# Kernel tuning notes

Hardware: AMD Instinct MI355X
Metric: run time of the kernel (lower is better)

## Reference

```python
import jax, jax.numpy as jnp
import numpy as np
import math

V, T, D, H, L, B = 50257, 1024, 768, 12, 6, 2
FF = 4 * D
HD = D // H

def layernorm(x, g, b, eps=1e-5):
    mu = jnp.mean(x, axis=-1, keepdims=True)
    var = jnp.var(x, axis=-1, keepdims=True)
    return (x - mu) * jax.lax.rsqrt(var + eps) * g + b

def new_gelu(x):
    # Faithful to the (buggy) NewGelu: tanh arg = sqrt(2/pi) * 0.044715 * x**4
    c = math.sqrt(2.0 / math.pi)
    return 0.5 * x * (1.0 + jnp.tanh(c * (x * 0.044715 * jnp.power(x, 3))))

def setup_inputs() -> dict:
    key = jax.random.key(0)
    ks = jax.random.split(key, 18)
    n = lambda k, shape, s=0.02: (jax.random.normal(k, shape, dtype=jnp.float32) * s)
    return {
        "ids": jax.random.randint(ks[0], (B, T), 0, V),
        "wte": n(ks[1], (V, D)),
        "wpe": n(ks[2], (T, D)),
        "W_qkv": n(ks[3], (L, D, 3 * D)),
        "b_qkv": jnp.zeros((L, 3 * D), jnp.float32),
        "W_o": n(ks[4], (L, D, D)),
        "b_o": jnp.zeros((L, D), jnp.float32),
        "ln1_g": jnp.ones((L, D), jnp.float32),
        "ln1_b": jnp.zeros((L, D), jnp.float32),
        "W1": n(ks[5], (L, D, FF)),
        "b1": jnp.zeros((L, FF), jnp.float32),
        "W2": n(ks[6], (L, FF, D)),
        "b2": jnp.zeros((L, D), jnp.float32),
        "lnf_g": jnp.ones((D,), jnp.float32),
        "lnf_b": jnp.zeros((D,), jnp.float32),
        "W_head": n(ks[7], (D, V)),
        "b_head": jnp.zeros((V,), jnp.float32),
    }

def reference(ids, wte, wpe, W_qkv, b_qkv, W_o, b_o, ln1_g, ln1_b,
              W1, b1, W2, b2, lnf_g, lnf_b, W_head, b_head):
    t = ids.shape[1]
    x = wte[ids] + wpe[:t][None]  # [B,T,D]
    scale = 1.0 / math.sqrt(HD)
    for l in range(L):
        qkv = x @ W_qkv[l] + b_qkv[l]                 # [B,T,3D]
        q, k, v = jnp.split(qkv, 3, axis=-1)
        q = q.reshape(-1, t, H, HD).transpose(0, 2, 1, 3)  # [B,H,T,hd]
        k = k.reshape(-1, t, H, HD).transpose(0, 2, 1, 3)
        v = v.reshape(-1, t, H, HD).transpose(0, 2, 1, 3)
        # NOTE: mask buffer is all-ones in the source, so NO causal masking.
        att = jax.nn.softmax(jnp.einsum('bhqd,bhkd->bhqk', q, k) * scale, axis=-1)
        y = jnp.einsum('bhqk,bhkd->bhqd', att, v)
        y = y.transpose(0, 2, 1, 3).reshape(-1, t, D)
        y = y @ W_o[l] + b_o[l]
        x = layernorm(y, ln1_g[l], ln1_b[l]) + x      # ln1 AFTER attn, per source
        h = new_gelu(x @ W1[l] + b1[l]) @ W2[l] + b2[l]  # ln2 unused, per source
        x = h + x
    x = layernorm(x, lnf_g, lnf_b)
    logits = x @ W_head + b_head
    return logits
```

## Files before the change

kernel.cpp:

```cpp
#include <hip/hip_runtime.h>
#include <hip/hip_bf16.h>
#include <math.h>
#include <stdint.h>

#define NL 6
#define NB 2
#define ST 1024
#define ND 768
#define NH 12
#define HD 64
#define NFF 3072
#define NV 50257
#define ND3 2304
#define NM (NB * ST)

typedef short bf16x4 __attribute__((ext_vector_type(4)));
typedef short bf16x8 __attribute__((ext_vector_type(8)));
typedef float f32x4  __attribute__((ext_vector_type(4)));

typedef __attribute__((address_space(3))) void as3_void;
typedef __attribute__((address_space(1))) void as1_void;

__device__ __forceinline__ void async_copy16(const void* g, void* lds) {
  __builtin_amdgcn_global_load_lds((const as1_void*)(uintptr_t)g,
                                   (as3_void*)(uint32_t)(uintptr_t)lds,
                                   16, 0, 0);
}

__device__ __forceinline__ unsigned short f2bf(float f) {
  union { float f; uint32_t u; } v; v.f = f;
  return (unsigned short)((v.u + 0x7fffu + ((v.u >> 16) & 1u)) >> 16);
}

__device__ __forceinline__ bf16x8 frag16(const unsigned short* p) {
  return *(const bf16x8*)p;
}

template <int N>
__device__ __forceinline__ void wait_vm_barrier() {
  if constexpr (N == 8)      asm volatile("s_waitcnt vmcnt(8)\n\ts_barrier" ::: "memory");
  else if constexpr (N == 6) asm volatile("s_waitcnt vmcnt(6)\n\ts_barrier" ::: "memory");
  else if constexpr (N == 5) asm volatile("s_waitcnt vmcnt(5)\n\ts_barrier" ::: "memory");
  else if constexpr (N == 4) asm volatile("s_waitcnt vmcnt(4)\n\ts_barrier" ::: "memory");
  else                       asm volatile("s_waitcnt vmcnt(0)\n\ts_barrier" ::: "memory");
}
__device__ __forceinline__ void lgkm_barrier() {
  asm volatile("s_waitcnt lgkmcnt(0)\n\ts_barrier" ::: "memory");
}

#define MFMA(a, b, c) __builtin_amdgcn_mfma_f32_16x16x32_bf16((a), (b), (c), 0, 0, 0)

__device__ __forceinline__ float gelu_buggy(float x) {
  const float c = 0.7978845608028654f;
  float x2 = x * x;
  return 0.5f * x * (1.0f + tanhf(c * 0.044715f * x2 * x2));
}

enum { EP_QKV = 0, EP_PROJ, EP_FF1, EP_FF2, EP_HEAD };

template <int EPI, int TM, int TN, int WN, int NW, int BK, int NBUF>
__global__ __launch_bounds__(NW * 64)
void gemm_bt(const unsigned short* __restrict__ A,
             const unsigned short* __restrict__ BT,
             const float* __restrict__ bias,
             float* __restrict__ Cf,
             unsigned short* __restrict__ Cb,
             const float* __restrict__ resid,
             unsigned short* __restrict__ vT,
             int M, int N, int K)
{
  constexpr int WM = NW / WN;
  constexpr int FM = TM / WM / 16;
  constexpr int FN = TN / WN / 16;
  constexpr int SL = BK / 8;
  constexpr int RS = (BK == 32) ? 1 : 0;
  constexpr int RPC = 1024 / (BK * 2);
  constexpr int CA = TM / RPC / NW;
  constexpr int CB = TN / RPC / NW;
  constexpr int LPT = CA + CB;
  constexpr int KK = BK / 32;
  constexpr int DEPTH = NBUF - 1;
  __shared__ __align__(16) unsigned short As[NBUF][TM * BK];
  __shared__ __align__(16) unsigned short Bs[NBUF][TN * BK];
  const int tid = threadIdx.x;
  const int w = tid >> 6, l = tid & 63;
  const int g = l >> 4, r = l & 15;
  const int wm = (w / WN) * (FM * 16);
  const int wn = (w % WN) * (FN * 16);

  const int nbx = gridDim.x;
  const int nwg = nbx * gridDim.y;
  int bid = blockIdx.y * nbx + blockIdx.x;
  if ((nwg & 7) == 0) bid = (bid & 7) * (nwg >> 3) + (bid >> 3);
  const int m0 = (bid % nbx) * TM, n0 = (bid / nbx) * TN;

  const int sr = l / (BK / 8);
  const int se = ((l & (SL - 1)) ^ ((sr >> RS) & (SL - 1))) * 8;
  long aoff[CA];
  long boff[CB];
#pragma unroll
  for (int c = 0; c < CA; ++c) {
    const int arow = (w * CA + c) * RPC + sr;
    aoff[c] = (long)(m0 + arow) * K + se;
  }
#pragma unroll
  for (int c = 0; c < CB; ++c) {
    int brow = n0 + (w * CB + c) * RPC + sr;
    if (brow > N - 1) brow = N - 1;
    boff[c] = (long)brow * K + se;
  }

  f32x4 acc[FM][FN] = {};

  auto stage = [&](int t, int buf) {
    const long k0 = (long)t * BK;
#pragma unroll
    for (int c = 0; c < CA; ++c)
      async_copy16(A + aoff[c] + k0, &As[buf][(w * CA + c) * 512]);
#pragma unroll
    for (int c = 0; c < CB; ++c)
      async_copy16(BT + boff[c] + k0, &Bs[buf][(w * CB + c) * 512]);
  };

  auto compute = [&](int buf) {
#pragma unroll
    for (int kk = 0; kk < KK; ++kk) {
      bf16x8 af[FM], bf[FN];
#pragma unroll
      for (int mi = 0; mi < FM; ++mi)
        af[mi] = frag16(&As[buf][(wm + mi * 16 + r) * BK +
                                 (((kk * 4 + g) ^ ((r >> RS) & (SL - 1))) * 8)]);
#pragma unroll
      for (int ni = 0; ni < FN; ++ni)
        bf[ni] = frag16(&Bs[buf][(wn + ni * 16 + r) * BK +
                                 (((kk * 4 + g) ^ ((r >> RS) & (SL - 1))) * 8)]);
      __builtin_amdgcn_s_setprio(1);
#pragma unroll
      for (int mi = 0; mi < FM; ++mi)
#pragma unroll
        for (int ni = 0; ni < FN; ++ni)
          acc[mi][ni] = MFMA(af[mi], bf[ni], acc[mi][ni]);
      __builtin_amdgcn_s_setprio(0);
    }
  };

  const int nt = K / BK;
  stage(0, 0);
  if (DEPTH == 2) stage(1, 1);
  int cur = 0, nxt = DEPTH;
  for (int t = 0; t < nt; ++t) {
    const bool have_next = (t + DEPTH) < nt;
    if (have_next) stage(t + DEPTH, nxt);
    if (have_next && DEPTH == 2)       wait_vm_barrier<2 * LPT>();
    else if (have_next || (DEPTH == 2 && t + 1 < nt)) wait_vm_barrier<LPT>();
    else                               wait_vm_barrier<0>();
    compute(cur);
    if (t + 1 < nt) lgkm_barrier();
    cur = (cur + 1 == NBUF) ? 0 : cur + 1;
    nxt = (nxt + 1 == NBUF) ? 0 : nxt + 1;
  }

#pragma unroll
  for (int mi = 0; mi < FM; ++mi) {
#pragma unroll
    for (int ni = 0; ni < FN; ++ni) {
      const int col = n0 + wn + ni * 16 + r;
      const float bb = bias[col];
      if (EPI == EP_QKV && col >= 2 * ND) {
        const int hv = (col - 2 * ND) >> 6, d = (col - 2 * ND) & 63;
        short4 vv;
#pragma unroll
        for (int q = 0; q < 4; ++q)
          vv[q] = (short)f2bf(acc[mi][ni][q] + bb);
        const int row = m0 + wm + mi * 16 + g * 4;
        const int bb_ = row >> 10, t4 = row & 1023;
        *(short4*)&vT[(((long)bb_ * NH + hv) * HD + d) * ST + t4] = vv;
        continue;
      }
#pragma unroll
      for (int q = 0; q < 4; ++q) {
        const int row = m0 + wm + mi * 16 + g * 4 + q;
        float v = acc[mi][ni][q] + bb;
        if constexpr (EPI == EP_QKV) {
          Cb[(long)row * N + col] = f2bf(v);
        } else if constexpr (EPI == EP_PROJ) {
          Cf[(long)row * N + col] = v;
        } else if constexpr (EPI == EP_FF1) {
          Cb[(long)row * N + col] = f2bf(gelu_buggy(v));
        } else if constexpr (EPI == EP_FF2) {
          float o = v + resid[(long)row * N + col];
          Cf[(long)row * N + col] = o;
          Cb[(long)row * N + col] = f2bf(o);
        }
      }
    }
  }
}

__global__ __launch_bounds__(512, 2)
void gemm_head_8ph(const unsigned short* __restrict__ A,
                   const unsigned short* __restrict__ BT,
                   const float* __restrict__ bias,
                   float* __restrict__ Cf,
                   int M, int N, int K)
{
  __shared__ __align__(16) unsigned short As[2][256 * 64];
  __shared__ __align__(16) unsigned short Bs[2][256 * 64];
  const int tid = threadIdx.x;
  const int w = tid >> 6, l = tid & 63;
  const int g = l >> 4, r = l & 15;
  const int wm = (w >> 2) * 128;
  const int wn = (w & 3) * 64;

  const int nbx = gridDim.x;
  const int nwg = nbx * gridDim.y;
  int bid = blockIdx.y * nbx + blockIdx.x;
  bid = (bid & 7) * (nwg >> 3) + (bid >> 3);
  const int m0 = (bid % nbx) * 256, n0 = (bid / nbx) * 256;

  const int sr = l >> 3;
  const int se = ((l & 7) ^ sr) * 8;
  const int a_base0 = (w < 4 ? 0 : 128) + (w & 3) * 8;

  auto stageA = [&](int tt, int q) {
    const int row = a_base0 + q * 32;
    async_copy16(A + (long)(m0 + row + sr) * K + tt * 64 + se,
                 &As[tt & 1][row * 64]);
  };
  auto stageB = [&](int tt, int h) {
#pragma unroll
    for (int c = 0; c < 2; ++c) {
      const int row = h * 128 + w * 16 + c * 8;
      int brow = n0 + row + sr; if (brow > N - 1) brow = N - 1;
      async_copy16(BT + (long)brow * K + tt * 64 + se,
                   &Bs[tt & 1][row * 64]);
    }
  };
  auto ldA = [&](int buf, int mi, int kk) -> bf16x8 {
    const int row = wm + mi * 16 + r;
    return frag16(&As[buf][row * 64 + (((kk * 4 + g) ^ (r & 7)) * 8)]);
  };
  auto ldB = [&](int buf, int ni, int kk) -> bf16x8 {
    const int row = wn + ni * 16 + r;
    return frag16(&Bs[buf][row * 64 + (((kk * 4 + g) ^ (r & 7)) * 8)]);
  };

  f32x4 acc[8][4] = {};
  bf16x8 bfr[4][2];

#define DO_PHASE(buf, p, first)                                           \
  do {                                                                    \
    bf16x8 af[2][2];                                                      \
    _Pragma("unroll")                                                     \
    for (int i_ = 0; i_ < 2; ++i_)                                        \
      _Pragma("unroll")                                                   \
      for (int k_ = 0; k_ < 2; ++k_)                                      \
        af[i_][k_] = ldA(buf, 2 * (p) + i_, k_);                          \
    if (first) {                                                          \
      _Pragma("unroll")                                                   \
      for (int n_ = 0; n_ < 4; ++n_)                                      \
        _Pragma("unroll")                                                 \
        for (int k_ = 0; k_ < 2; ++k_)                                    \
          bfr[n_][k_] = ldB(buf, n_, k_);                                 \
    }                                                                     \
    asm volatile("s_barrier" ::: "memory");                               \
    asm volatile("s_waitcnt lgkmcnt(0)" ::: "memory");                    \
    __builtin_amdgcn_sched_barrier(0);                                    \
    __builtin_amdgcn_s_setprio(1);                                        \
    _Pragma("unroll")                                                     \
    for (int i_ = 0; i_ < 2; ++i_)                                        \
      _Pragma("unroll")                                                   \
      for (int n_ = 0; n_ < 4; ++n_)                                      \
        _Pragma("unroll")                                                 \
        for (int k_ = 0; k_ < 2; ++k_)                                    \
          acc[2 * (p) + i_][n_] =                                         \
              MFMA(af[i_][k_], bfr[n_][k_], acc[2 * (p) + i_][n_]);       \
    __builtin_amdgcn_s_setprio(0);                                        \
    asm volatile("s_barrier" ::: "memory");                               \
  } while (0)

  const int nt = K >> 6;
  const int niter = nt >> 1;

#pragma unroll
  for (int q = 0; q < 4; ++q) stageA(0, q);
  stageB(0, 0); stageB(0, 1);
#pragma unroll
  for (int q = 0; q < 4; ++q) stageA(1, q);
  stageB(1, 0); stageB(1, 1);

  for (int it = 0; it < niter; ++it) {
    const int T = 2 * it;
    if (it > 0) { stageA(T + 1, 3); stageB(T + 1, 0); }
    if (it == 0) wait_vm_barrier<8>(); else wait_vm_barrier<5>();
    DO_PHASE(0, 0, true);
    if (T + 2 < nt) stageA(T + 2, 0);
    if (it > 0) stageB(T + 1, 1);
    DO_PHASE(0, 1, false);
    if (T + 2 < nt) stageA(T + 2, 1);
    DO_PHASE(0, 2, false);
    if (T + 2 < nt) stageA(T + 2, 2);
    DO_PHASE(0, 3, false);
    if (T + 2 < nt) { stageA(T + 2, 3); stageB(T + 2, 0); }
    if (it == 0) wait_vm_barrier<6>();
    else if (it == niter - 1) wait_vm_barrier<0>();
    else wait_vm_barrier<5>();
    DO_PHASE(1, 0, true);
    if (T + 3 < nt) stageA(T + 3, 0);
    if (T + 2 < nt) stageB(T + 2, 1);
    DO_PHASE(1, 1, false);
    if (T + 3 < nt) stageA(T + 3, 1);
    DO_PHASE(1, 2, false);
    if (T + 3 < nt) stageA(T + 3, 2);
    DO_PHASE(1, 3, false);
  }
#undef DO_PHASE

#pragma unroll
  for (int mi = 0; mi < 8; ++mi) {
#pragma unroll
    for (int ni = 0; ni < 4; ++ni) {
      const int col = n0 + wn + ni * 16 + r;
      if (col >= N) continue;
      const float bb = bias[col];
#pragma unroll
      for (int q = 0; q < 4; ++q) {
        const int row = m0 + wm + mi * 16 + g * 4 + q;
        Cf[(long)row * N + col] = acc[mi][ni][q] + bb;
      }
    }
  }
}

__global__ __launch_bounds__(256)
void attn_kernel(const unsigned short* __restrict__ qkv,
                 const unsigned short* __restrict__ vT,
                 unsigned short* __restrict__ y)
{
  constexpr int LS = 72;
  __shared__ __align__(16) unsigned short Qs[64 * LS];
  __shared__ __align__(16) unsigned short Ks[64 * LS];
  __shared__ __align__(16) unsigned short Vt[64 * LS];
  __shared__ __align__(16) unsigned short Ps[64 * LS];
  const int tid = threadIdx.x;
  const int w = tid >> 6, l = tid & 63;
  const int g = l >> 4, r = l & 15;
  const int q0 = blockIdx.x * 64;
  const int b = blockIdx.y / NH, h = blockIdx.y % NH;
  const long rb = (long)b * ST;
  const long vbase = ((long)b * NH + h) * HD * ST;
  const int srow = tid >> 3, sc8 = (tid & 7) * 8;

#pragma unroll
  for (int p = 0; p < 2; ++p) {
    const int row = p * 32 + srow;
    bf16x8 v = *(const bf16x8*)&qkv[(rb + q0 + row) * ND3 + h * HD + sc8];
    *(bf16x8*)&Qs[row * LS + sc8] = v;
  }
  __syncthreads();
  bf16x8 aq[2];
#pragma unroll
  for (int kk = 0; kk < 2; ++kk)
    aq[kk] = *(const bf16x8*)&Qs[(w * 16 + r) * LS + kk * 32 + g * 8];

  float m_run[4] = {-1e30f, -1e30f, -1e30f, -1e30f};
  float l_run[4] = {0.f, 0.f, 0.f, 0.f};
  f32x4 acc_o[4] = {};

  for (int kt = 0; kt < ST / 64; ++kt) {
#pragma unroll
    for (int p = 0; p < 2; ++p) {
      const int row = p * 32 + srow;
      *(bf16x8*)&Ks[row * LS + sc8] =
          *(const bf16x8*)&qkv[(rb + kt * 64 + row) * ND3 + ND + h * HD + sc8];
      *(bf16x8*)&Vt[row * LS + sc8] =
          *(const bf16x8*)&vT[vbase + (long)row * ST + kt * 64 + sc8];
    }
    __syncthreads();

    f32x4 s_acc[4] = {};
#pragma unroll
    for (int kk = 0; kk < 2; ++kk) {
#pragma unroll
      for (int ni = 0; ni < 4; ++ni) {
        bf16x8 bk = *(const bf16x8*)&Ks[(ni * 16 + r) * LS + kk * 32 + g * 8];
        s_acc[ni] = MFMA(aq[kk], bk, s_acc[ni]);
      }
    }

    float mloc[4];
#pragma unroll
    for (int q = 0; q < 4; ++q) {
      float mx = fmaxf(fmaxf(s_acc[0][q], s_acc[1][q]), fmaxf(s_acc[2][q], s_acc[3][q]));
      mloc[q] = mx * 0.125f;
    }
#pragma unroll
    for (int mask = 1; mask < 16; mask <<= 1)
#pragma unroll
      for (int q = 0; q < 4; ++q)
        mloc[q] = fmaxf(mloc[q], __shfl_xor(mloc[q], mask, 64));

    float alpha[4], psum[4] = {0.f, 0.f, 0.f, 0.f};
#pragma unroll
    for (int q = 0; q < 4; ++q) {
      const float mn = fmaxf(m_run[q], mloc[q]);
      alpha[q] = __expf(m_run[q] - mn);
      m_run[q] = mn;
    }
#pragma unroll
    for (int ni = 0; ni < 4; ++ni)
#pragma unroll
      for (int q = 0; q < 4; ++q) {
        const float p = __expf(s_acc[ni][q] * 0.125f - m_run[q]);
        psum[q] += p;
        Ps[(w * 16 + g * 4 + q) * LS + ni * 16 + r] = f2bf(p);
      }
#pragma unroll
    for (int mask = 1; mask < 16; mask <<= 1)
#pragma unroll
      for (int q = 0; q < 4; ++q) psum[q] += __shfl_xor(psum[q], mask, 64);
#pragma unroll
    for (int q = 0; q < 4; ++q) l_run[q] = l_run[q] * alpha[q] + psum[q];
#pragma unroll
    for (int ni = 0; ni < 4; ++ni)
#pragma unroll
      for (int q = 0; q < 4; ++q) acc_o[ni][q] *= alpha[q];

    asm volatile("s_waitcnt lgkmcnt(0)" ::: "memory");
    __builtin_amdgcn_sched_barrier(0);

#pragma unroll
    for (int kk = 0; kk < 2; ++kk) {
      bf16x8 ap = *(const bf16x8*)&Ps[(w * 16 + r) * LS + kk * 32 + g * 8];
#pragma unroll
      for (int ni = 0; ni < 4; ++ni) {
        bf16x8 bv = *(const bf16x8*)&Vt[(ni * 16 + r) * LS + kk * 32 + g * 8];
        acc_o[ni] = MFMA(ap, bv, acc_o[ni]);
      }
    }
    __syncthreads();
  }

#pragma unroll
  for (int ni = 0; ni < 4; ++ni)
#pragma unroll
    for (int q = 0; q < 4; ++q) {
      const int row = q0 + w * 16 + g * 4 + q;
      const int col = h * HD + ni * 16 + r;
      y[(rb + row) * ND + col] = f2bf(acc_o[ni][q] / l_run[q]);
    }
}

template <bool RESID>
__global__ __launch_bounds__(256)
void ln_kernel(const float* __restrict__ in, const float* __restrict__ resid,
               const float* __restrict__ gamma, const float* __restrict__ beta,
               float* __restrict__ out_f, unsigned short* __restrict__ out_b)
{
  __shared__ float wred[8];
  const int row = blockIdx.x, tid = threadIdx.x;
  float v[3];
#pragma unroll
  for (int j = 0; j < 3; ++j) v[j] = in[(long)row * ND + tid + j * 256];
  float s = v[0] + v[1] + v[2];
#pragma unroll
  for (int m = 1; m < 64; m <<= 1) s += __shfl_xor(s, m, 64);
  if ((tid & 63) == 0) wred[tid >> 6] = s;
  __syncthreads();
  const float mean = (wred[0] + wred[1] + wred[2] + wred[3]) * (1.0f / ND);
  float d[3];
#pragma unroll
  for (int j = 0; j < 3; ++j) d[j] = v[j] - mean;
  float s2 = d[0] * d[0] + d[1] * d[1] + d[2] * d[2];
#pragma unroll
  for (int m = 1; m < 64; m <<= 1) s2 += __shfl_xor(s2, m, 64);
  if ((tid & 63) == 0) wred[4 + (tid >> 6)] = s2;
  __syncthreads();
  const float var = (wred[4] + wred[5] + wred[6] + wred[7]) * (1.0f / ND);
  const float rstd = rsqrtf(var + 1e-5f);
#pragma unroll
  for (int j = 0; j < 3; ++j) {
    const int c = tid + j * 256;
    float o = d[j] * rstd * gamma[c] + beta[c];
    if (RESID) o += resid[(long)row * ND + c];
    if (out_f) out_f[(long)row * ND + c] = o;
    if (out_b) out_b[(long)row * ND + c] = f2bf(o);
  }
}

__global__ __launch_bounds__(256)
void embed_kernel(const int* __restrict__ ids, const float* __restrict__ wte,
                  const float* __restrict__ wpe, float* __restrict__ x,
                  unsigned short* __restrict__ xb)
{
  const int t = blockIdx.x, tid = threadIdx.x;
  const int tok = ids[t];
  const int pos = t & (ST - 1);
#pragma unroll
  for (int j = 0; j < 3; ++j) {
    const int c = tid + j * 256;
    const float v = wte[(long)tok * ND + c] + wpe[(long)pos * ND + c];
    x[(long)t * ND + c] = v;
    xb[(long)t * ND + c] = f2bf(v);
  }
}

__global__ __launch_bounds__(256)
void transpose_bf16(const float* __restrict__ in, unsigned short* __restrict__ out,
                    int R, int C)
{
  __shared__ float tile[64][33];
  const long z = (long)blockIdx.z * R * C;
  const int c0 = blockIdx.x * 32, r0 = blockIdx.y * 64;
  const int tx = threadIdx.x & 31, ty = threadIdx.x >> 5;
#pragma unroll
  for (int j = 0; j < 8; ++j) {
    const int rr = r0 + j * 8 + ty, cc = c0 + tx;
    if (cc < C) tile[j * 8 + ty][tx] = in[z + (long)rr * C + cc];
  }
  __syncthreads();
  const int rx = threadIdx.x & 63, cy = threadIdx.x >> 6;
#pragma unroll
  for (int j = 0; j < 8; ++j) {
    const int cc = c0 + j * 4 + cy;
    if (cc < C) out[z + (long)cc * R + r0 + rx] = f2bf(tile[rx][j * 4 + cy]);
  }
}

extern "C" void kernel_launch(void* const* d_in, const int* in_sizes, int n_in,
                              void* d_out, int out_size, void* d_ws, size_t ws_size,
                              hipStream_t stream)
{
  const int*   ids    = (const int*)d_in[0];
  const float* wte    = (const float*)d_in[1];
  const float* wpe    = (const float*)d_in[2];
  const float* W_qkv  = (const float*)d_in[3];
  const float* b_qkv  = (const float*)d_in[4];
  const float* W_o    = (const float*)d_in[5];
  const float* b_o    = (const float*)d_in[6];
  const float* ln1_g  = (const float*)d_in[7];
  const float* ln1_b  = (const float*)d_in[8];
  const float* W1     = (const float*)d_in[9];
  const float* b1     = (const float*)d_in[10];
  const float* W2     = (const float*)d_in[11];
  const float* b2     = (const float*)d_in[12];
  const float* lnf_g  = (const float*)d_in[13];
  const float* lnf_b  = (const float*)d_in[14];
  const float* W_head = (const float*)d_in[15];
  const float* b_head = (const float*)d_in[16];
  float* out = (float*)d_out;
  (void)in_sizes; (void)n_in; (void)out_size; (void)ws_size;

  char* ws = (char*)d_ws;
  size_t off = 0;
  auto alloc = [&](size_t bytes) -> void* {
    void* p = (void*)(ws + off);
    off = (off + bytes + 255) & ~(size_t)255;
    return p;
  };
  unsigned short* wqkvT = (unsigned short*)alloc((size_t)NL * ND3 * ND * 2);
  unsigned short* woT   = (unsigned short*)alloc((size_t)NL * ND * ND * 2);
  unsigned short* w1T   = (unsigned short*)alloc((size_t)NL * NFF * ND * 2);
  unsigned short* w2T   = (unsigned short*)alloc((size_t)NL * ND * NFF * 2);
  unsigned short* whT   = (unsigned short*)alloc((size_t)NV * ND * 2);
  float*          xf    = (float*)alloc((size_t)NM * ND * 4);
  unsigned short* xb    = (unsigned short*)alloc((size_t)NM * ND * 2);
  unsigned short* qkvb  = (unsigned short*)alloc((size_t)NM * ND3 * 2);
  unsigned short* yb    = (unsigned short*)alloc((size_t)NM * ND * 2);
  float*          aof   = (float*)alloc((size_t)NM * ND * 4);
  unsigned short* h1b   = (unsigned short*)alloc((size_t)NM * NFF * 2);
  unsigned short* xlnb  = (unsigned short*)alloc((size_t)NM * ND * 2);
  unsigned short* vtb   = (unsigned short*)alloc((size_t)NB * NH * HD * ST * 2);

  dim3 tb(256);
  dim3 tb128(128);
  dim3 tb512(512);
  transpose_bf16<<<dim3(ND3 / 32, ND / 64, NL), tb, 0, stream>>>(W_qkv, wqkvT, ND, ND3);
  transpose_bf16<<<dim3(ND / 32, ND / 64, NL), tb, 0, stream>>>(W_o, woT, ND, ND);
  transpose_bf16<<<dim3(NFF / 32, ND / 64, NL), tb, 0, stream>>>(W1, w1T, ND, NFF);
  transpose_bf16<<<dim3(ND / 32, NFF / 64, NL), tb, 0, stream>>>(W2, w2T, NFF, ND);
  transpose_bf16<<<dim3((NV + 31) / 32, ND / 64, 1), tb, 0, stream>>>(W_head, whT, ND, NV);

  embed_kernel<<<dim3(NM), tb, 0, stream>>>(ids, wte, wpe, xf, xb);

  for (int l = 0; l < NL; ++l) {
    gemm_bt<EP_QKV, 128, 64, 2, 4, 64, 2><<<dim3(NM / 128, ND3 / 64), tb, 0, stream>>>(
        xb, wqkvT + (size_t)l * ND3 * ND, b_qkv + (size_t)l * ND3,
        nullptr, qkvb, nullptr, vtb, NM, ND3, ND);
    attn_kernel<<<dim3(ST / 64, NB * NH), tb, 0, stream>>>(qkvb, vtb, yb);
    gemm_bt<EP_PROJ, 64, 64, 2, 2, 64, 2><<<dim3(NM / 64, ND / 64), tb128, 0, stream>>>(
        yb, woT + (size_t)l * ND * ND, b_o + (size_t)l * ND,
        aof, nullptr, nullptr, nullptr, NM, ND, ND);
    ln_kernel<true><<<dim3(NM), tb, 0, stream>>>(
        aof, xf, ln1_g + (size_t)l * ND, ln1_b + (size_t)l * ND, xf, xb);
    gemm_bt<EP_FF1, 128, 64, 2, 4, 64, 2><<<dim3(NM / 128, NFF / 64), tb, 0, stream>>>(
        xb, w1T + (size_t)l * NFF * ND, b1 + (size_t)l * NFF,
        nullptr, h1b, nullptr, nullptr, NM, NFF, ND);
    gemm_bt<EP_FF2, 64, 64, 2, 2, 64, 2><<<dim3(NM / 64, ND / 64), tb128, 0, stream>>>(
        h1b, w2T + (size_t)l * ND * NFF, b2 + (size_t)l * ND,
        xf, xb, xf, nullptr, NM, ND, NFF);
  }
  ln_kernel<false><<<dim3(NM), tb, 0, stream>>>(xf, nullptr, lnf_g, lnf_b, nullptr, xlnb);
  gemm_head_8ph<<<dim3(NM / 256, (NV + 255) / 256), tb512, 0, stream>>>(
      xlnb, whT, b_head, out, NM, NV, ND);
}
```

Before: 1.105 ms.

## Enlarge QKV/FF1 GEMM tiles, add occupancy hint, use wave-per-row layernorm

Switches the QKV and FF1 GEMMs from 128x64 tiles with BK=64 to 128x128 tiles with BK=32. This raises operand reuse and halves the grid. It also adds a min-blocks-per-CU hint of 2 to the GEMM launch bounds and new vmcnt wait variants. The layernorm kernel is rewritten so each wavefront handles one row with shuffle-only reductions, removing the LDS round trips and __syncthreads. Risks are more register pressure from the launch-bounds hint and fewer blocks on the QKV/FF1 grids.

```diff
diff --git a/kernel.cpp b/kernel.cpp
--- a/kernel.cpp
+++ b/kernel.cpp
@@ -42,6 +42,8 @@
   else if constexpr (N == 6) asm volatile("s_waitcnt vmcnt(6)\n\ts_barrier" ::: "memory");
   else if constexpr (N == 5) asm volatile("s_waitcnt vmcnt(5)\n\ts_barrier" ::: "memory");
   else if constexpr (N == 4) asm volatile("s_waitcnt vmcnt(4)\n\ts_barrier" ::: "memory");
+  else if constexpr (N == 3) asm volatile("s_waitcnt vmcnt(3)\n\ts_barrier" ::: "memory");
+  else if constexpr (N == 2) asm volatile("s_waitcnt vmcnt(2)\n\ts_barrier" ::: "memory");
   else                       asm volatile("s_waitcnt vmcnt(0)\n\ts_barrier" ::: "memory");
 }
 __device__ __forceinline__ void lgkm_barrier() {
@@ -59,7 +61,7 @@
 enum { EP_QKV = 0, EP_PROJ, EP_FF1, EP_FF2, EP_HEAD };
 
 template <int EPI, int TM, int TN, int WN, int NW, int BK, int NBUF>
-__global__ __launch_bounds__(NW * 64)
+__global__ __launch_bounds__(NW * 64, 2)
 void gemm_bt(const unsigned short* __restrict__ A,
              const unsigned short* __restrict__ BT,
              const float* __restrict__ bias,
@@ -457,31 +459,28 @@
                const float* __restrict__ gamma, const float* __restrict__ beta,
                float* __restrict__ out_f, unsigned short* __restrict__ out_b)
 {
-  __shared__ float wred[8];
-  const int row = blockIdx.x, tid = threadIdx.x;
-  float v[3];
-#pragma unroll
-  for (int j = 0; j < 3; ++j) v[j] = in[(long)row * ND + tid + j * 256];
-  float s = v[0] + v[1] + v[2];
+  const int w = threadIdx.x >> 6, l = threadIdx.x & 63;
+  const int row = blockIdx.x * 4 + w;
+  const float* p = in + (long)row * ND;
+  float v[12];
+#pragma unroll
+  for (int j = 0; j < 12; ++j) v[j] = p[l + j * 64];
+  float s = 0.f;
+#pragma unroll
+  for (int j = 0; j < 12; ++j) s += v[j];
 #pragma unroll
   for (int m = 1; m < 64; m <<= 1) s += __shfl_xor(s, m, 64);
-  if ((tid & 63) == 0) wred[tid >> 6] = s;
-  __syncthreads();
-  const float mean = (wred[0] + wred[1] + wred[2] + wred[3]) * (1.0f / ND);
-  float d[3];
-#pragma unroll
-  for (int j = 0; j < 3; ++j) d[j] = v[j] - mean;
-  float s2 = d[0] * d[0] + d[1] * d[1] + d[2] * d[2];
+  const float mean = s * (1.0f / ND);
+  float s2 = 0.f;
+#pragma unroll
+  for (int j = 0; j < 12; ++j) { v[j] -= mean; s2 += v[j] * v[j]; }
 #pragma unroll
   for (int m = 1; m < 64; m <<= 1) s2 += __shfl_xor(s2, m, 64);
-  if ((tid & 63) == 0) wred[4 + (tid >> 6)] = s2;
-  __syncthreads();
-  const float var = (wred[4] + wred[5] + wred[6] + wred[7]) * (1.0f / ND);
-  const float rstd = rsqrtf(var + 1e-5f);
-#pragma unroll
-  for (int j = 0; j < 3; ++j) {
-    const int c = tid + j * 256;
-    float o = d[j] * rstd * gamma[c] + beta[c];
+  const float rstd = rsqrtf(s2 * (1.0f / ND) + 1e-5f);
+#pragma unroll
+  for (int j = 0; j < 12; ++j) {
+    const int c = l + j * 64;
+    float o = v[j] * rstd * gamma[c] + beta[c];
     if (RESID) o += resid[(long)row * ND + c];
     if (out_f) out_f[(long)row * ND + c] = o;
     if (out_b) out_b[(long)row * ND + c] = f2bf(o);
@@ -584,23 +583,23 @@
   embed_kernel<<<dim3(NM), tb, 0, stream>>>(ids, wte, wpe, xf, xb);
 
   for (int l = 0; l < NL; ++l) {
-    gemm_bt<EP_QKV, 128, 64, 2, 4, 64, 2><<<dim3(NM / 128, ND3 / 64), tb, 0, stream>>>(
+    gemm_bt<EP_QKV, 128, 128, 2, 4, 32, 2><<<dim3(NM / 128, ND3 / 128), tb, 0, stream>>>(
         xb, wqkvT + (size_t)l * ND3 * ND, b_qkv + (size_t)l * ND3,
         nullptr, qkvb, nullptr, vtb, NM, ND3, ND);
     attn_kernel<<<dim3(ST / 64, NB * NH), tb, 0, stream>>>(qkvb, vtb, yb);
     gemm_bt<EP_PROJ, 64, 64, 2, 2, 64, 2><<<dim3(NM / 64, ND / 64), tb128, 0, stream>>>(
         yb, woT + (size_t)l * ND * ND, b_o + (size_t)l * ND,
         aof, nullptr, nullptr, nullptr, NM, ND, ND);
-    ln_kernel<true><<<dim3(NM), tb, 0, stream>>>(
+    ln_kernel<true><<<dim3(NM / 4), tb, 0, stream>>>(
         aof, xf, ln1_g + (size_t)l * ND, ln1_b + (size_t)l * ND, xf, xb);
-    gemm_bt<EP_FF1, 128, 64, 2, 4, 64, 2><<<dim3(NM / 128, NFF / 64), tb, 0, stream>>>(
+    gemm_bt<EP_FF1, 128, 128, 2, 4, 32, 2><<<dim3(NM / 128, NFF / 128), tb, 0, stream>>>(
         xb, w1T + (size_t)l * NFF * ND, b1 + (size_t)l * NFF,
         nullptr, h1b, nullptr, nullptr, NM, NFF, ND);
     gemm_bt<EP_FF2, 64, 64, 2, 2, 64, 2><<<dim3(NM / 64, ND / 64), tb128, 0, stream>>>(
         h1b, w2T + (size_t)l * ND * NFF, b2 + (size_t)l * ND,
         xf, xb, xf, nullptr, NM, ND, NFF);
   }
-  ln_kernel<false><<<dim3(NM), tb, 0, stream>>>(xf, nullptr, lnf_g, lnf_b, nullptr, xlnb);
+  ln_kernel<false><<<dim3(NM / 4), tb, 0, stream>>>(xf, nullptr, lnf_g, lnf_b, nullptr, xlnb);
   gemm_head_8ph<<<dim3(NM / 256, (NV + 255) / 256), tb512, 0, stream>>>(
       xlnb, whT, b_head, out, NM, NV, ND);
 }
```

Result: slower. 1.189 ms (+7.6%).
